# Performance work log

Measured on AMD Instinct MI355X. Metric: run time of the kernel, lower is better.

## Reference

```python
import jax, jax.numpy as jnp
import numpy as np

DIM = 2048
N_HEADS = 16
N_KV_HEADS = 4
HEAD_DIM = DIM // N_HEADS


def setup_inputs() -> dict:
    key = jax.random.key(0)
    k1, k2, k3, k4, k5 = jax.random.split(key, 5)
    B, T = 2, 2048
    scale = 1.0 / np.sqrt(DIM)
    x = jax.random.normal(k1, (B, T, DIM), dtype=jnp.float32)
    # weights stored as [in, out] so forward is x @ W (same math as nn.Linear)
    Wq = jax.random.normal(k2, (DIM, DIM), dtype=jnp.float32) * scale
    Wk = jax.random.normal(k3, (DIM, N_KV_HEADS * HEAD_DIM), dtype=jnp.float32) * scale
    Wv = jax.random.normal(k4, (DIM, N_KV_HEADS * HEAD_DIM), dtype=jnp.float32) * scale
    Wo = jax.random.normal(k5, (DIM, DIM), dtype=jnp.float32) * scale
    return {"x": x, "Wq": Wq, "Wk": Wk, "Wv": Wv, "Wo": Wo}


def reference(x, Wq, Wk, Wv, Wo):
    B, T, C = x.shape
    G = N_HEADS // N_KV_HEADS  # query heads per kv head
    # projections
    q = (x @ Wq).reshape(B, T, N_KV_HEADS, G, HEAD_DIM)   # [B,T,K,G,d]
    k = (x @ Wk).reshape(B, T, N_KV_HEADS, HEAD_DIM)      # [B,T,K,d]
    v = (x @ Wv).reshape(B, T, N_KV_HEADS, HEAD_DIM)      # [B,T,K,d]
    # attention scores: grouped heads share kv head (no repeat_interleave copy)
    att = jnp.einsum('btkgd,bskd->bkgts', q, k) / np.sqrt(HEAD_DIM)  # [B,K,G,T,T]
    att = jax.nn.softmax(att, axis=-1)
    out = jnp.einsum('bkgts,bskd->btkgd', att, v).reshape(B, T, C)
    return out @ Wo
```

## Files before the change

kernel.cpp:

```cpp
#include <hip/hip_runtime.h>
#include <hip/hip_bf16.h>

typedef __hip_bfloat16 bf16;
typedef __attribute__((ext_vector_type(8))) short short8;
typedef __attribute__((ext_vector_type(4))) short short4v;
typedef __attribute__((ext_vector_type(4))) float f32x4;

#define DIMC 2048
#define TSEQ 2048
#define NB 2
#define KVH 4
#define NH 16
#define HD 128
#define KVD 512
#define QSCALE 0.12751744f

__device__ __forceinline__ void mfma16(f32x4& acc, short8 a, short8 b) {
  acc = __builtin_amdgcn_mfma_f32_16x16x32_bf16(a, b, acc, 0, 0, 0);
}

__device__ __forceinline__ void gload_lds16(const bf16* g, bf16* l) {
  __builtin_amdgcn_global_load_lds(
      (const __attribute__((address_space(1))) void*)g,
      (__attribute__((address_space(3))) void*)l, 16, 0, 0);
}

__device__ __forceinline__ int swz(int row, int col) {
  return col ^ ((row & 7) << 3);
}

__global__ __launch_bounds__(256) void f2b(const float* __restrict__ in,
                                           bf16* __restrict__ out, long n4) {
  long i = (long)blockIdx.x * 256 + threadIdx.x;
  if (i >= n4) return;
  const f32x4 v = *(const f32x4*)(in + i * 4);
  union { short4v s; bf16 h[4]; } u;
#pragma unroll
  for (int j = 0; j < 4; ++j) u.h[j] = __float2bfloat16(v[j]);
  *(short4v*)(out + i * 4) = u.s;
}

__global__ __launch_bounds__(256) void transpose_w_f2b(const float* __restrict__ in,
                                                       bf16* __restrict__ out, int C,
                                                       float scale) {
  __shared__ bf16 tile[64][72];
  int rb = blockIdx.y * 64, cb = blockIdx.x * 64;
  int tx = threadIdx.x & 63, ty = threadIdx.x >> 6;
  for (int i = ty; i < 64; i += 4)
    tile[i][tx] = __float2bfloat16(in[(long)(rb + i) * C + cb + tx] * scale);
  __syncthreads();
  for (int i = ty; i < 64; i += 4)
    out[(long)(cb + i) * DIMC + rb + tx] = tile[tx][i];
}

#define GEMM_BODY(A_, Bt_, K_)                                                  \
  const int tid = threadIdx.x;                                                  \
  const int lane = tid & 63, wid = tid >> 6;                                    \
  const long m0 = blockIdx.y * 128, n0 = blockIdx.x * 128;                      \
  const int wm = (wid >> 1) * 64, wn = (wid & 1) * 64;                          \
  f32x4 acc[4][4] = {};                                                         \
  const int srow = lane >> 2, scol = (lane & 3) * 8;                            \
  const bf16* Ag = A_ + (m0 + srow) * (long)K_ + scol;                          \
  const bf16* Bg = Bt_ + (n0 + srow) * (long)K_ + scol;                         \
  for (int k0 = 0; k0 < K_; k0 += 32) {                                         \
    for (int p = 0; p < 2; ++p) {                                               \
      int rr = p * 64 + wid * 16;                                               \
      gload_lds16(Ag + (long)rr * K_ + k0, As + rr * 32);                       \
      gload_lds16(Bg + (long)rr * K_ + k0, Bs + rr * 32);                       \
    }                                                                           \
    __syncthreads();                                                            \
    const int ko = (lane >> 4) * 8;                                             \
    short8 af[4], bq[4];                                                        \
    _Pragma("unroll") for (int i = 0; i < 4; ++i) {                             \
      af[i] = *(const short8*)(As + (wm + i * 16 + (lane & 15)) * 32 + ko);     \
      bq[i] = *(const short8*)(Bs + (wn + i * 16 + (lane & 15)) * 32 + ko);     \
    }                                                                           \
    _Pragma("unroll") for (int i = 0; i < 4; ++i)                               \
      _Pragma("unroll") for (int j = 0; j < 4; ++j)                             \
        mfma16(acc[i][j], af[i], bq[j]);                                        \
    __syncthreads();                                                            \
  }                                                                             \
  const int cr = (lane >> 4) * 4, cc = lane & 15;

__global__ __launch_bounds__(256) void gemm_qkv(const bf16* __restrict__ A,
                                                const bf16* __restrict__ Bt,
                                                bf16* __restrict__ qp,
                                                bf16* __restrict__ kp,
                                                bf16* __restrict__ vT) {
  __shared__ bf16 As[128 * 32];
  __shared__ bf16 Bs[128 * 32];
  GEMM_BODY(A, Bt, 2048)
#pragma unroll
  for (int i = 0; i < 4; ++i)
#pragma unroll
    for (int j = 0; j < 4; ++j)
#pragma unroll
      for (int r = 0; r < 4; ++r) {
        long m = m0 + wm + i * 16 + cr + r;
        long n = n0 + wn + j * 16 + cc;
        float val = acc[i][j][r];
        if (n0 < 2048) {
          qp[m * DIMC + n] = __float2bfloat16(val);
        } else if (n0 < 2560) {
          kp[m * KVD + (n - 2048)] = __float2bfloat16(val);
        } else {
          long nn = n - 2560;
          long z = (m >> 11) * 4 + (nn >> 7);
          vT[z * (HD * (long)TSEQ) + (nn & 127) * (long)TSEQ + (m & 2047)] =
              __float2bfloat16(val);
        }
      }
}

__global__ __launch_bounds__(256) void gemm_out(const bf16* __restrict__ A,
                                                const bf16* __restrict__ Bt,
                                                float* __restrict__ C) {
  __shared__ bf16 As[128 * 32];
  __shared__ bf16 Bs[128 * 32];
  GEMM_BODY(A, Bt, 2048)
#pragma unroll
  for (int i = 0; i < 4; ++i)
#pragma unroll
    for (int j = 0; j < 4; ++j)
#pragma unroll
      for (int r = 0; r < 4; ++r) {
        long m = m0 + wm + i * 16 + cr + r;
        long n = n0 + wn + j * 16 + cc;
        C[m * DIMC + n] = acc[i][j][r];
      }
}

__global__ __launch_bounds__(512, 4) void attn_fwd(const bf16* __restrict__ Qp,
                                                   const bf16* __restrict__ Kp,
                                                   const bf16* __restrict__ Vt,
                                                   bf16* __restrict__ AO) {
  __shared__ bf16 Ks[64 * 128];
  __shared__ bf16 Vts[128 * 64];
  const int tid = threadIdx.x;
  const int lane = tid & 63, wid = tid >> 6;
  const int h = blockIdx.y, b = blockIdx.z;
  const int kv = h >> 2;
  const int t0 = blockIdx.x * 128;
  const int lr = lane & 15, lg = lane >> 4;

  short8 aq[4];
  {
    const bf16* qrow =
        Qp + ((long)(b * TSEQ + t0 + wid * 16 + lr)) * DIMC + h * HD + lg * 8;
#pragma unroll
    for (int c = 0; c < 4; ++c) aq[c] = *(const short8*)(qrow + c * 32);
  }
  f32x4 o[8] = {};
  float mrun = -1e30f, lrun = 0.f;

  const bf16* Kg = Kp + (long)b * TSEQ * KVD + kv * HD;
  const bf16* Vg = Vt + ((long)(b * KVH + kv)) * HD * TSEQ;

  const int krow = tid >> 3, kc0 = (tid & 7) * 16;
  const int vrow = tid >> 2, va = tid & 3;
  short8 kreg[2], vreg[2];
#pragma unroll
  for (int p = 0; p < 2; ++p) {
    kreg[p] = *(const short8*)(Kg + (long)krow * KVD + kc0 + p * 8);
    vreg[p] = *(const short8*)(Vg + (long)vrow * TSEQ + (va + 4 * p) * 8);
  }

  for (int s0 = 0; s0 < TSEQ; s0 += 64) {
    __syncthreads();
#pragma unroll
    for (int p = 0; p < 2; ++p) {
      *(short8*)(Ks + krow * 128 + swz(krow, kc0 + p * 8)) = kreg[p];
      *(short8*)(Vts + vrow * 64 + ((va + 4 * p + vrow) & 7) * 8) = vreg[p];
    }
    __syncthreads();
    if (s0 + 64 < TSEQ) {
#pragma unroll
      for (int p = 0; p < 2; ++p) {
        kreg[p] = *(const short8*)(Kg + (long)(s0 + 64 + krow) * KVD + kc0 + p * 8);
        vreg[p] = *(const short8*)(Vg + (long)vrow * TSEQ + s0 + 64 + (va + 4 * p) * 8);
      }
    }

    f32x4 sacc[4] = {};
#pragma unroll
    for (int sf = 0; sf < 4; ++sf)
#pragma unroll
      for (int c = 0; c < 4; ++c) {
        int row = sf * 16 + lr;
        short8 kf = *(const short8*)(Ks + row * 128 + swz(row, c * 32 + lg * 8));
        mfma16(sacc[sf], kf, aq[c]);
      }

    float tmax = sacc[0][0];
#pragma unroll
    for (int sf = 0; sf < 4; ++sf)
#pragma unroll
      for (int r = 0; r < 4; ++r) tmax = fmaxf(tmax, sacc[sf][r]);
    tmax = fmaxf(tmax, __shfl_xor(tmax, 16));
    tmax = fmaxf(tmax, __shfl_xor(tmax, 32));
    if (__any(tmax > mrun)) {
      float mnew = fmaxf(mrun, tmax);
      float fac = exp2f(mrun - mnew);
      mrun = mnew;
      lrun *= fac;
#pragma unroll
      for (int df = 0; df < 8; ++df) o[df] *= fac;
    }
    float p4[4][4];
    float ps = 0.f;
#pragma unroll
    for (int sf = 0; sf < 4; ++sf)
#pragma unroll
      for (int r = 0; r < 4; ++r) {
        float pv = exp2f(sacc[sf][r] - mrun);
        p4[sf][r] = pv;
        ps += pv;
      }
    ps += __shfl_xor(ps, 16);
    ps += __shfl_xor(ps, 32);
    lrun += ps;

    union { short8 s; bf16 h[8]; } pb[2];
#pragma unroll
    for (int c2 = 0; c2 < 2; ++c2)
#pragma unroll
      for (int r = 0; r < 4; ++r) {
        pb[c2].h[r] = __float2bfloat16(p4[2 * c2][r]);
        pb[c2].h[4 + r] = __float2bfloat16(p4[2 * c2 + 1][r]);
      }

#pragma unroll
    for (int c2 = 0; c2 < 2; ++c2) {
      const int l0 = 4 * c2 + (lg >> 1), w0 = (lg & 1) * 4;
#pragma unroll
      for (int df = 0; df < 8; ++df) {
        int row = df * 16 + lr;
        union { short8 s; short4v q[2]; } vf;
        vf.q[0] = *(const short4v*)(Vts + row * 64 + ((l0 + row) & 7) * 8 + w0);
        vf.q[1] = *(const short4v*)(Vts + row * 64 + ((l0 + 2 + row) & 7) * 8 + w0);
        mfma16(o[df], vf.s, pb[c2].s);
      }
    }
  }

  float inv = 1.0f / lrun;
  bf16* obase =
      AO + ((long)(b * TSEQ + t0 + wid * 16 + lr)) * DIMC + h * HD + lg * 4;
#pragma unroll
  for (int df = 0; df < 8; ++df) {
    union { short4v s; bf16 h[4]; } ov;
#pragma unroll
    for (int r = 0; r < 4; ++r) ov.h[r] = __float2bfloat16(o[df][r] * inv);
    *(short4v*)(obase + df * 16) = ov.s;
  }
}

extern "C" void kernel_launch(void* const* d_in, const int* in_sizes, int n_in,
                              void* d_out, int out_size, void* d_ws, size_t ws_size,
                              hipStream_t stream) {
  const float* x  = (const float*)d_in[0];
  const float* Wq = (const float*)d_in[1];
  const float* Wk = (const float*)d_in[2];
  const float* Wv = (const float*)d_in[3];
  const float* Wo = (const float*)d_in[4];
  float* out = (float*)d_out;
  bf16* ws = (bf16*)d_ws;

  bf16* xb  = ws;
  bf16* WT3 = xb + 8388608;
  bf16* qp  = WT3 + 6291456;
  bf16* kp  = qp + 8388608;
  bf16* vT  = kp + 2097152;

  f2b<<<8192, 256, 0, stream>>>(x, xb, 2097152);
  transpose_w_f2b<<<dim3(32, 32), 256, 0, stream>>>(Wq, WT3, 2048, QSCALE);
  transpose_w_f2b<<<dim3(8, 32), 256, 0, stream>>>(Wk, WT3 + (long)2048 * 2048, 512, 1.0f);
  transpose_w_f2b<<<dim3(8, 32), 256, 0, stream>>>(Wv, WT3 + (long)2560 * 2048, 512, 1.0f);

  gemm_qkv<<<dim3(24, 32), 256, 0, stream>>>(xb, WT3, qp, kp, vT);

  transpose_w_f2b<<<dim3(32, 32), 256, 0, stream>>>(Wo, WT3, 2048, 1.0f);

  bf16* ao = xb;
  attn_fwd<<<dim3(16, 16, 2), 512, 0, stream>>>(qp, kp, vT, ao);

  gemm_out<<<dim3(16, 32), 256, 0, stream>>>(ao, WT3, out);
}
```

Before: 271.3 us.

## Split attention over key sequence into two halves with a combine kernel

Adds a split-KV (flash-decoding style) path: each attention block processes only half of the key sequence, doubling the grid to 1024 blocks, and writes unnormalized partial outputs plus running max and sum. A new combine kernel merges the two halves with rescaling. This targets low occupancy or tail imbalance on a GPU with many CUs, since 512 blocks may underfill the device. In exchange it costs extra workspace traffic for the bf16 partials, an additional launch, and an extra rounding of the partial outputs to bf16. The old path is kept as a fallback when the workspace is too small.

```diff
diff --git a/kernel.cpp b/kernel.cpp
--- a/kernel.cpp
+++ b/kernel.cpp
@@ -130,15 +130,22 @@
       }
 }
 
+template <bool PARTIAL>
 __global__ __launch_bounds__(512, 4) void attn_fwd(const bf16* __restrict__ Qp,
                                                    const bf16* __restrict__ Kp,
                                                    const bf16* __restrict__ Vt,
-                                                   bf16* __restrict__ AO) {
+                                                   bf16* __restrict__ AO,
+                                                   bf16* __restrict__ op2,
+                                                   float* __restrict__ mlb) {
   __shared__ bf16 Ks[64 * 128];
   __shared__ bf16 Vts[128 * 64];
   const int tid = threadIdx.x;
   const int lane = tid & 63, wid = tid >> 6;
-  const int h = blockIdx.y, b = blockIdx.z;
+  const int h = blockIdx.y;
+  const int z = blockIdx.z;
+  const int b = PARTIAL ? (z >> 1) : z;
+  const int s_lo = PARTIAL ? (z & 1) * 1024 : 0;
+  const int s_hi = s_lo + (PARTIAL ? 1024 : 2048);
   const int kv = h >> 2;
   const int t0 = blockIdx.x * 128;
   const int lr = lane & 15, lg = lane >> 4;
@@ -161,11 +168,11 @@
   short8 kreg[2], vreg[2];
 #pragma unroll
   for (int p = 0; p < 2; ++p) {
-    kreg[p] = *(const short8*)(Kg + (long)krow * KVD + kc0 + p * 8);
-    vreg[p] = *(const short8*)(Vg + (long)vrow * TSEQ + (va + 4 * p) * 8);
-  }
-
-  for (int s0 = 0; s0 < TSEQ; s0 += 64) {
+    kreg[p] = *(const short8*)(Kg + (long)(s_lo + krow) * KVD + kc0 + p * 8);
+    vreg[p] = *(const short8*)(Vg + (long)vrow * TSEQ + s_lo + (va + 4 * p) * 8);
+  }
+
+  for (int s0 = s_lo; s0 < s_hi; s0 += 64) {
     __syncthreads();
 #pragma unroll
     for (int p = 0; p < 2; ++p) {
@@ -173,7 +180,7 @@
       *(short8*)(Vts + vrow * 64 + ((va + 4 * p + vrow) & 7) * 8) = vreg[p];
     }
     __syncthreads();
-    if (s0 + 64 < TSEQ) {
+    if (s0 + 64 < s_hi) {
 #pragma unroll
       for (int p = 0; p < 2; ++p) {
         kreg[p] = *(const short8*)(Kg + (long)(s0 + 64 + krow) * KVD + kc0 + p * 8);
@@ -243,16 +250,58 @@
     }
   }
 
-  float inv = 1.0f / lrun;
-  bf16* obase =
-      AO + ((long)(b * TSEQ + t0 + wid * 16 + lr)) * DIMC + h * HD + lg * 4;
-#pragma unroll
-  for (int df = 0; df < 8; ++df) {
-    union { short4v s; bf16 h[4]; } ov;
-#pragma unroll
-    for (int r = 0; r < 4; ++r) ov.h[r] = __float2bfloat16(o[df][r] * inv);
-    *(short4v*)(obase + df * 16) = ov.s;
-  }
+  if (PARTIAL) {
+    bf16* obase =
+        op2 + ((long)(z * TSEQ) + t0 + wid * 16 + lr) * DIMC + h * HD + lg * 4;
+#pragma unroll
+    for (int df = 0; df < 8; ++df) {
+      union { short4v s; bf16 h[4]; } ov;
+#pragma unroll
+      for (int r = 0; r < 4; ++r) ov.h[r] = __float2bfloat16(o[df][r]);
+      *(short4v*)(obase + df * 16) = ov.s;
+    }
+    if (lane < 16) {
+      long mi = ((long)z * TSEQ + t0 + wid * 16 + lr) * NH + h;
+      mlb[mi] = mrun;
+      mlb[(long)4 * TSEQ * NH + mi] = lrun;
+    }
+  } else {
+    float inv = 1.0f / lrun;
+    bf16* obase =
+        AO + ((long)(b * TSEQ + t0 + wid * 16 + lr)) * DIMC + h * HD + lg * 4;
+#pragma unroll
+    for (int df = 0; df < 8; ++df) {
+      union { short4v s; bf16 h[4]; } ov;
+#pragma unroll
+      for (int r = 0; r < 4; ++r) ov.h[r] = __float2bfloat16(o[df][r] * inv);
+      *(short4v*)(obase + df * 16) = ov.s;
+    }
+  }
+}
+
+__global__ __launch_bounds__(256) void attn_combine(const bf16* __restrict__ op2,
+                                                    const float* __restrict__ mlb,
+                                                    bf16* __restrict__ ao) {
+  long idx = (long)blockIdx.x * 256 + threadIdx.x;
+  int r = idx >> 8, c8 = idx & 255;
+  int b = r >> 11, t = r & 2047, h = c8 >> 4;
+  long z1 = b * 2, z2 = z1 + 1;
+  long m1i = (z1 * TSEQ + t) * NH + h, m2i = (z2 * TSEQ + t) * NH + h;
+  const long loff = (long)4 * TSEQ * NH;
+  float m1 = mlb[m1i], m2 = mlb[m2i];
+  float l1 = mlb[loff + m1i], l2 = mlb[loff + m2i];
+  float m = fmaxf(m1, m2);
+  float a1 = exp2f(m1 - m), a2 = exp2f(m2 - m);
+  float inv = 1.0f / (l1 * a1 + l2 * a2);
+  a1 *= inv; a2 *= inv;
+  union { short8 s; bf16 h[8]; } o1, o2, ov;
+  o1.s = *(const short8*)(op2 + (z1 * TSEQ + t) * DIMC + c8 * 8);
+  o2.s = *(const short8*)(op2 + (z2 * TSEQ + t) * DIMC + c8 * 8);
+#pragma unroll
+  for (int j = 0; j < 8; ++j)
+    ov.h[j] = __float2bfloat16(__bfloat162float(o1.h[j]) * a1 +
+                               __bfloat162float(o2.h[j]) * a2);
+  *(short8*)(ao + (long)r * DIMC + c8 * 8) = ov.s;
 }
 
 extern "C" void kernel_launch(void* const* d_in, const int* in_sizes, int n_in,
@@ -271,6 +320,9 @@
   bf16* qp  = WT3 + 6291456;
   bf16* kp  = qp + 8388608;
   bf16* vT  = kp + 2097152;
+  bf16* op2 = vT + 2097152;
+  float* mlb = (float*)(op2 + 16777216);
+  const size_t ws_needed = (size_t)(27262976 + 16777216) * 2 + 262144 * 4;
 
   f2b<<<8192, 256, 0, stream>>>(x, xb, 2097152);
   transpose_w_f2b<<<dim3(32, 32), 256, 0, stream>>>(Wq, WT3, 2048, QSCALE);
@@ -282,7 +334,12 @@
   transpose_w_f2b<<<dim3(32, 32), 256, 0, stream>>>(Wo, WT3, 2048, 1.0f);
 
   bf16* ao = xb;
-  attn_fwd<<<dim3(16, 16, 2), 512, 0, stream>>>(qp, kp, vT, ao);
+  if (ws_size >= ws_needed) {
+    attn_fwd<true><<<dim3(16, 16, 4), 512, 0, stream>>>(qp, kp, vT, ao, op2, mlb);
+    attn_combine<<<4096, 256, 0, stream>>>(op2, mlb, ao);
+  } else {
+    attn_fwd<false><<<dim3(16, 16, 2), 512, 0, stream>>>(qp, kp, vT, ao, op2, mlb);
+  }
 
   gemm_out<<<dim3(16, 32), 256, 0, stream>>>(ao, WT3, out);
 }
```

After: 281.8 us. +3.8%, slower.
